# Optimization experiments

Measured on AMD Instinct MI355X. Metric: run time of the kernel, lower is better.

The kernel has to match this reference:

```python
import jax, jax.numpy as jnp
import numpy as np

# Module hyperparameters (from init_kwargs)
KH, KW = 3, 3
STRIDE_H = STRIDE_W = 1
PAD_H = PAD_W = 1
DIL_H = DIL_W = 1
DEFORM_GROUPS = 1
IN_CH, OUT_CH = 64, 64


def setup_inputs() -> dict:
    key = jax.random.key(0)
    k1, k2, k3, k4 = jax.random.split(key, 4)
    B, C, H, W = 4, IN_CH, 128, 128
    K = KH * KW
    x = jax.random.normal(k1, (B, C, H, W), dtype=jnp.float32)
    offset = jax.random.normal(k2, (B, DEFORM_GROUPS * 2 * K, H, W), dtype=jnp.float32)
    mask = jax.random.uniform(k3, (B, DEFORM_GROUPS * K, H, W), dtype=jnp.float32)
    stdv = 1.0 / np.sqrt(C * KH * KW)
    weight = jax.random.uniform(k4, (OUT_CH, C, KH, KW), dtype=jnp.float32,
                                minval=-stdv, maxval=stdv)
    bias = jnp.zeros((OUT_CH,), dtype=jnp.float32)
    return {"x": x, "offset": offset, "mask": mask, "weight": weight, "bias": bias}


def _bilinear_gather(img, ys, xs):
    """img: [N,Cg,H,W]; ys,xs: [N,K,Ho,Wo] absolute pixel coords.
    Returns [N,K,Ho,Wo,Cg]; zero padding outside, matches torch grid_sample
    (align_corners=False, padding_mode='zeros')."""
    N, Cg, H, W = img.shape
    y0f = jnp.floor(ys)
    x0f = jnp.floor(xs)
    wy = (ys - y0f)[..., None]
    wx = (xs - x0f)[..., None]
    y0 = y0f.astype(jnp.int32)
    x0 = x0f.astype(jnp.int32)
    b = jnp.arange(N)[:, None, None, None]

    def g(yi, xi):
        valid = (yi >= 0) & (yi < H) & (xi >= 0) & (xi < W)
        v = img[b, :, jnp.clip(yi, 0, H - 1), jnp.clip(xi, 0, W - 1)]  # [N,K,Ho,Wo,Cg]
        return jnp.where(valid[..., None], v, jnp.zeros((), img.dtype))

    v00 = g(y0, x0)
    v01 = g(y0, x0 + 1)
    v10 = g(y0 + 1, x0)
    v11 = g(y0 + 1, x0 + 1)
    return (v00 * (1 - wy) * (1 - wx) + v01 * (1 - wy) * wx
            + v10 * wy * (1 - wx) + v11 * wy * wx)


def _mdcn(x, offset, mask, weight, bias):
    B, C, H, W = x.shape
    O = weight.shape[0]
    K = KH * KW
    G = DEFORM_GROUPS
    Cg = C // G
    Ho = (H + 2 * PAD_H - (DIL_H * (KH - 1) + 1)) // STRIDE_H + 1
    Wo = (W + 2 * PAD_W - (DIL_W * (KW - 1) + 1)) // STRIDE_W + 1

    base_y = jnp.arange(Ho, dtype=x.dtype) * STRIDE_H - PAD_H          # [Ho]
    base_x = jnp.arange(Wo, dtype=x.dtype) * STRIDE_W - PAD_W          # [Wo]
    ky = (jnp.arange(K) // KW).astype(x.dtype) * DIL_H                 # [K]
    kx = (jnp.arange(K) % KW).astype(x.dtype) * DIL_W                  # [K]

    off = offset.reshape(B, G, K, 2, Ho, Wo)
    sy = (base_y[None, None, None, :, None] + ky[None, None, :, None, None]
          + off[:, :, :, 0])                                           # [B,G,K,Ho,Wo]
    sx = (base_x[None, None, None, None, :] + kx[None, None, :, None, None]
          + off[:, :, :, 1])

    img = x.reshape(B * G, Cg, H, W)
    sampled = _bilinear_gather(img, sy.reshape(B * G, K, Ho, Wo),
                               sx.reshape(B * G, K, Ho, Wo))            # [B*G,K,Ho,Wo,Cg]
    sampled = sampled * mask.reshape(B * G, K, Ho, Wo)[..., None]
    sampled = sampled.reshape(B, G, K, Ho, Wo, Cg)

    w = weight.reshape(O, G, Cg, K)
    out = jnp.einsum('bgkhwc,ogck->bohw', sampled, w)
    return out + bias[None, :, None, None]


def reference(x, offset, mask, weight, bias):
    return _mdcn(x, offset, mask, weight, bias)
```

## Files before the change

### kernel.cpp

```cpp
#include <hip/hip_runtime.h>
#include <hip/hip_bf16.h>
#include <math.h>

constexpr int B = 4, C = 64, H = 128, W = 128, K = 9, O = 64;
constexpr int HXW = H * W;

typedef _Float16 half8 __attribute__((ext_vector_type(8)));
typedef float f32x4 __attribute__((ext_vector_type(4)));

__global__ void wt_kernel(const float* __restrict__ weight, float* __restrict__ wt) {
    int idx = blockIdx.x * 256 + threadIdx.x;
    if (idx >= K * C * O) return;
    int o = idx & 63;
    int c = (idx >> 6) & 63;
    int k = idx >> 12;
    wt[idx] = weight[(o * C + c) * K + k];
}

__global__ __launch_bounds__(256) void mdcn_nchw(
        const float* __restrict__ x, const float* __restrict__ offset,
        const float* __restrict__ mask, const float* __restrict__ wt,
        const float* __restrict__ bias, float* __restrict__ out) {
    int pid = blockIdx.x * 256 + threadIdx.x;
    int b = pid >> 14;
    int hw = pid & (HXW - 1);
    int h = hw >> 7;
    int w = hw & 127;
    float acc[O];
#pragma unroll
    for (int o = 0; o < O; ++o) acc[o] = bias[o];
#pragma unroll 1
    for (int k = 0; k < K; ++k) {
        float offy = offset[((size_t)(b * 2 * K + 2 * k)) * HXW + hw];
        float offx = offset[((size_t)(b * 2 * K + 2 * k + 1)) * HXW + hw];
        float m    = mask[((size_t)(b * K + k)) * HXW + hw];
        float sy = (float)(h - 1 + k / 3) + offy;
        float sx = (float)(w - 1 + k % 3) + offx;
        float y0f = floorf(sy), x0f = floorf(sx);
        float wy = sy - y0f, wx = sx - x0f;
        int y0 = (int)y0f, x0 = (int)x0f;
        int y1 = y0 + 1, x1 = x0 + 1;
        bool vy0 = (y0 >= 0) & (y0 < H), vy1 = (y1 >= 0) & (y1 < H);
        bool vx0 = (x0 >= 0) & (x0 < W), vx1 = (x1 >= 0) & (x1 < W);
        float w00 = (vy0 & vx0) ? (1.0f - wy) * (1.0f - wx) * m : 0.0f;
        float w01 = (vy0 & vx1) ? (1.0f - wy) * wx * m : 0.0f;
        float w10 = (vy1 & vx0) ? wy * (1.0f - wx) * m : 0.0f;
        float w11 = (vy1 & vx1) ? wy * wx * m : 0.0f;
        int y0c = min(max(y0, 0), H - 1), y1c = min(max(y1, 0), H - 1);
        int x0c = min(max(x0, 0), W - 1), x1c = min(max(x1, 0), W - 1);
        const float* p00 = x + (size_t)b * C * HXW + y0c * W + x0c;
        const float* p01 = x + (size_t)b * C * HXW + y0c * W + x1c;
        const float* p10 = x + (size_t)b * C * HXW + y1c * W + x0c;
        const float* p11 = x + (size_t)b * C * HXW + y1c * W + x1c;
        const float* wk = wt + k * C * O;
#pragma unroll 1
        for (int c0 = 0; c0 < C; c0 += 4) {
            float v[4];
#pragma unroll
            for (int j = 0; j < 4; ++j) {
                size_t cs = (size_t)(c0 + j) * HXW;
                v[j] = w00 * p00[cs] + w01 * p01[cs] + w10 * p10[cs] + w11 * p11[cs];
            }
            const float* wr = wk + c0 * O;
#pragma unroll
            for (int j = 0; j < 4; ++j)
#pragma unroll
                for (int o = 0; o < O; ++o) acc[o] = fmaf(wr[j * O + o], v[j], acc[o]);
        }
    }
#pragma unroll
    for (int o = 0; o < O; ++o) out[((size_t)(b * O + o)) * HXW + hw] = acc[o];
}

constexpr int XT_BLOCKS = B * HXW / 128;
__global__ __launch_bounds__(256) void prep_kernel(
        const float* __restrict__ x, const float* __restrict__ weight,
        _Float16* __restrict__ xht, _Float16* __restrict__ wth) {
    int bid = blockIdx.x;
    if (bid < XT_BLOCKS) {
        __shared__ float lds[128 * 65];
        int t = threadIdx.x;
        int P = bid * 128;
        int b = P >> 14;
        int hw0 = P & (HXW - 1);
        int px = t & 127;
        int hf = t >> 7;
        const float* src = x + (size_t)b * C * HXW + hw0 + px;
#pragma unroll
        for (int cc = 0; cc < 32; ++cc) {
            int ch = hf * 32 + cc;
            lds[px * 65 + ch] = src[(size_t)ch * HXW];
        }
        __syncthreads();
        _Float16* dst = xht + ((size_t)b * HXW + hw0 + px) * 64 + hf * 32;
        const float* row = lds + px * 65 + hf * 32;
#pragma unroll
        for (int j = 0; j < 4; ++j) {
            half8 pk;
#pragma unroll
            for (int e = 0; e < 8; ++e) pk[e] = (_Float16)row[j * 8 + e];
            *(half8*)(dst + j * 8) = pk;
        }
    } else {
        int idx = (bid - XT_BLOCKS) * 256 + threadIdx.x;
        if (idx < K * O * C) {
            int e = idx & 7;
            int lane = (idx >> 3) & 63;
            int s = (idx >> 9) & 7;
            int k = idx >> 12;
            int ml = lane & 15, kg = lane >> 4;
            int nf = s & 3, ks = s >> 2;
            int o = nf * 16 + ml;
            int c = ks * 32 + kg * 8 + e;
            wth[idx] = (_Float16)weight[(o * C + c) * K + k];
        }
    }
}

__global__ __launch_bounds__(256, 4) void mdcn_f16(
        const _Float16* __restrict__ xht,
        const float* __restrict__ offset,
        const float* __restrict__ mask,
        const _Float16* __restrict__ wth,
        const float* __restrict__ bias,
        float* __restrict__ out) {
    __shared__ _Float16 Alds[4][16 * 64];

    int bid = blockIdx.x;
    int slab = bid & 7;
    int within = bid >> 3;
    int tid = threadIdx.x;
    int lane = tid & 63;
    int wid = tid >> 6;
    int ml = lane & 15, kg = lane >> 4;
    int p8 = lane >> 3, ch8 = lane & 7;
    int b = slab >> 1;
    int hwbase = (slab & 1) * 8192 + within * 64;
    int h = hwbase >> 7;
    int wvpx = wid * 16;
    int wbase = (hwbase & 127) + wvpx;
    _Float16* Aw = &Alds[wid][0];

    f32x4 acc[4];
#pragma unroll
    for (int nf = 0; nf < 4; ++nf) {
        float bv = bias[nf * 16 + ml];
        acc[nf] = (f32x4){bv, bv, bv, bv};
    }

    const _Float16* xb = xht + (size_t)b * HXW * 64;
    const float* offb = offset + (size_t)b * 2 * K * HXW;
    const float* mskb = mask + (size_t)b * K * HXW;

    float oy[2], ox[2], mm[2];
#pragma unroll
    for (int g = 0; g < 2; ++g) {
        int hw = hwbase + wvpx + g * 8 + p8;
        oy[g] = offb[hw];
        ox[g] = offb[(size_t)HXW + hw];
        mm[g] = mskb[hw];
    }

#pragma unroll 1
    for (int k = 0; k < K; ++k) {
        int ky = k / 3 - 1, kx = k % 3 - 1;

        float w00[2], w01[2], w10[2], w11[2];
        int r00[2], r01[2], r10[2], r11[2];
#pragma unroll
        for (int g = 0; g < 2; ++g) {
            int pl = g * 8 + p8;
            int w = wbase + pl;
            float sy = (float)(h + ky) + oy[g];
            float sx = (float)(w + kx) + ox[g];
            float y0f = floorf(sy), x0f = floorf(sx);
            float wy = sy - y0f, wx = sx - x0f;
            int y0 = (int)y0f, x0 = (int)x0f;
            int y1 = y0 + 1, x1 = x0 + 1;
            bool vy0 = (y0 >= 0) & (y0 < H), vy1 = (y1 >= 0) & (y1 < H);
            bool vx0 = (x0 >= 0) & (x0 < W), vx1 = (x1 >= 0) & (x1 < W);
            float m = mm[g];
            w00[g] = (vy0 & vx0) ? (1.0f - wy) * (1.0f - wx) * m : 0.0f;
            w01[g] = (vy0 & vx1) ? (1.0f - wy) * wx * m : 0.0f;
            w10[g] = (vy1 & vx0) ? wy * (1.0f - wx) * m : 0.0f;
            w11[g] = (vy1 & vx1) ? wy * wx * m : 0.0f;
            int y0c = min(max(y0, 0), H - 1), y1c = min(max(y1, 0), H - 1);
            int x0c = min(max(x0, 0), W - 1), x1c = min(max(x1, 0), W - 1);
            r00[g] = y0c * W + x0c;
            r01[g] = y0c * W + x1c;
            r10[g] = y1c * W + x0c;
            r11[g] = y1c * W + x1c;
        }

        half8 c00[2], c01[2], c10[2], c11[2];
#pragma unroll
        for (int g = 0; g < 2; ++g) {
            c00[g] = *(const half8*)(xb + r00[g] * 64 + ch8 * 8);
            c01[g] = *(const half8*)(xb + r01[g] * 64 + ch8 * 8);
            c10[g] = *(const half8*)(xb + r10[g] * 64 + ch8 * 8);
            c11[g] = *(const half8*)(xb + r11[g] * 64 + ch8 * 8);
        }

        float oy2[2], ox2[2], mm2[2];
        if (k + 1 < K) {
#pragma unroll
            for (int g = 0; g < 2; ++g) {
                int hw = hwbase + wvpx + g * 8 + p8;
                oy2[g] = offb[(size_t)(2 * k + 2) * HXW + hw];
                ox2[g] = offb[(size_t)(2 * k + 3) * HXW + hw];
                mm2[g] = mskb[(size_t)(k + 1) * HXW + hw];
            }
        }
        __builtin_amdgcn_sched_barrier(0);

#pragma unroll
        for (int g = 0; g < 2; ++g) {
            int pl = g * 8 + p8;
            _Float16 h00 = (_Float16)w00[g], h01 = (_Float16)w01[g];
            _Float16 h10 = (_Float16)w10[g], h11 = (_Float16)w11[g];
            half8 pk = c00[g] * h00 + c01[g] * h01 + c10[g] * h10 + c11[g] * h11;
            *(half8*)(Aw + pl * 64 + ((ch8 ^ (pl & 7)) * 8)) = pk;
        }

#pragma unroll
        for (int ks = 0; ks < 2; ++ks) {
            half8 bfr[4];
#pragma unroll
            for (int nf = 0; nf < 4; ++nf)
                bfr[nf] = *(const half8*)(wth + ((size_t)((k * 8 + ks * 4 + nf) * 64 + lane)) * 8);
            half8 af = *(const half8*)(Aw + ml * 64 + (((ks * 4 + kg) ^ (ml & 7)) * 8));
#pragma unroll
            for (int nf = 0; nf < 4; ++nf)
                acc[nf] = __builtin_amdgcn_mfma_f32_16x16x32_f16(af, bfr[nf], acc[nf], 0, 0, 0);
        }

        if (k + 1 < K) {
#pragma unroll
            for (int g = 0; g < 2; ++g) { oy[g] = oy2[g]; ox[g] = ox2[g]; mm[g] = mm2[g]; }
        }
    }

    int hwb = hwbase + wvpx + kg * 4;
#pragma unroll
    for (int nf = 0; nf < 4; ++nf) {
        size_t ob = ((size_t)(b * O + nf * 16 + ml)) * HXW + hwb;
        *(float4*)(out + ob) = __builtin_bit_cast(float4, acc[nf]);
    }
}

extern "C" void kernel_launch(void* const* d_in, const int* in_sizes, int n_in,
                              void* d_out, int out_size, void* d_ws, size_t ws_size,
                              hipStream_t stream) {
    const float* x      = (const float*)d_in[0];
    const float* offset = (const float*)d_in[1];
    const float* mask   = (const float*)d_in[2];
    const float* weight = (const float*)d_in[3];
    const float* bias   = (const float*)d_in[4];
    float* out = (float*)d_out;

    _Float16* wth = (_Float16*)d_ws;
    _Float16* xht = (_Float16*)((char*)d_ws + 73728);
    size_t need = 73728 + (size_t)B * HXW * 64 * sizeof(_Float16);

    if (ws_size >= need) {
        int wth_blocks = (K * O * C + 255) / 256;
        prep_kernel<<<XT_BLOCKS + wth_blocks, 256, 0, stream>>>(x, weight, xht, wth);
        mdcn_f16<<<1024, 256, 0, stream>>>(xht, offset, mask, wth, bias, out);
    } else {
        float* wt = (float*)d_ws;
        wt_kernel<<<(K * C * O + 255) / 256, 256, 0, stream>>>(weight, wt);
        mdcn_nchw<<<(B * HXW) / 256, 256, 0, stream>>>(x, offset, mask, wt, bias, out);
    }
}
```

Before: 39.42 us.

## Stage all weights in LDS and build MFMA A fragments in registers

Each 512-thread block now copies the full fp16 weight tensor (72KB) into shared memory once and reads B fragments from LDS instead of global memory. The per-wave LDS round trip for the sampled A tile is removed: each lane computes bilinear coordinates for its own pixel and gathers the channel slices that match its MFMA A-fragment layout directly. Blocks now cover a whole 128-pixel row, with half as many blocks of twice the size. The trade-offs are 72KB of LDS per block, which limits occupancy, and a prologue that loads every weight per block. Each pixel's coordinate math is also repeated across four lanes.

```diff
diff --git a/kernel.cpp b/kernel.cpp
--- a/kernel.cpp
+++ b/kernel.cpp
@@ -117,14 +117,14 @@
     }
 }
 
-__global__ __launch_bounds__(256, 4) void mdcn_f16(
+__global__ __launch_bounds__(512, 4) void mdcn_f16(
         const _Float16* __restrict__ xht,
         const float* __restrict__ offset,
         const float* __restrict__ mask,
         const _Float16* __restrict__ wth,
         const float* __restrict__ bias,
         float* __restrict__ out) {
-    __shared__ _Float16 Alds[4][16 * 64];
+    __shared__ _Float16 Wlds[K * 8 * 64 * 8];
 
     int bid = blockIdx.x;
     int slab = bid & 7;
@@ -133,13 +133,20 @@
     int lane = tid & 63;
     int wid = tid >> 6;
     int ml = lane & 15, kg = lane >> 4;
-    int p8 = lane >> 3, ch8 = lane & 7;
     int b = slab >> 1;
-    int hwbase = (slab & 1) * 8192 + within * 64;
-    int h = hwbase >> 7;
+    int row = (slab & 1) * 64 + within;
+    int hwrow = row * 128;
     int wvpx = wid * 16;
-    int wbase = (hwbase & 127) + wvpx;
-    _Float16* Aw = &Alds[wid][0];
+    int h = row;
+    int hwpx = hwrow + wvpx + ml;
+    int wpx = wvpx + ml;
+
+#pragma unroll
+    for (int j = 0; j < 9; ++j) {
+        int idx = tid + j * 512;
+        *(half8*)(Wlds + idx * 8) = *(const half8*)(wth + idx * 8);
+    }
+    __syncthreads();
 
     f32x4 acc[4];
 #pragma unroll
@@ -152,95 +159,70 @@
     const float* offb = offset + (size_t)b * 2 * K * HXW;
     const float* mskb = mask + (size_t)b * K * HXW;
 
-    float oy[2], ox[2], mm[2];
-#pragma unroll
-    for (int g = 0; g < 2; ++g) {
-        int hw = hwbase + wvpx + g * 8 + p8;
-        oy[g] = offb[hw];
-        ox[g] = offb[(size_t)HXW + hw];
-        mm[g] = mskb[hw];
-    }
+    float oy = offb[hwpx];
+    float ox = offb[(size_t)HXW + hwpx];
+    float mm = mskb[hwpx];
 
 #pragma unroll 1
     for (int k = 0; k < K; ++k) {
         int ky = k / 3 - 1, kx = k % 3 - 1;
 
-        float w00[2], w01[2], w10[2], w11[2];
-        int r00[2], r01[2], r10[2], r11[2];
-#pragma unroll
-        for (int g = 0; g < 2; ++g) {
-            int pl = g * 8 + p8;
-            int w = wbase + pl;
-            float sy = (float)(h + ky) + oy[g];
-            float sx = (float)(w + kx) + ox[g];
-            float y0f = floorf(sy), x0f = floorf(sx);
-            float wy = sy - y0f, wx = sx - x0f;
-            int y0 = (int)y0f, x0 = (int)x0f;
-            int y1 = y0 + 1, x1 = x0 + 1;
-            bool vy0 = (y0 >= 0) & (y0 < H), vy1 = (y1 >= 0) & (y1 < H);
-            bool vx0 = (x0 >= 0) & (x0 < W), vx1 = (x1 >= 0) & (x1 < W);
-            float m = mm[g];
-            w00[g] = (vy0 & vx0) ? (1.0f - wy) * (1.0f - wx) * m : 0.0f;
-            w01[g] = (vy0 & vx1) ? (1.0f - wy) * wx * m : 0.0f;
-            w10[g] = (vy1 & vx0) ? wy * (1.0f - wx) * m : 0.0f;
-            w11[g] = (vy1 & vx1) ? wy * wx * m : 0.0f;
-            int y0c = min(max(y0, 0), H - 1), y1c = min(max(y1, 0), H - 1);
-            int x0c = min(max(x0, 0), W - 1), x1c = min(max(x1, 0), W - 1);
-            r00[g] = y0c * W + x0c;
-            r01[g] = y0c * W + x1c;
-            r10[g] = y1c * W + x0c;
-            r11[g] = y1c * W + x1c;
-        }
+        float sy = (float)(h + ky) + oy;
+        float sx = (float)(wpx + kx) + ox;
+        float y0f = floorf(sy), x0f = floorf(sx);
+        float wy = sy - y0f, wx = sx - x0f;
+        int y0 = (int)y0f, x0 = (int)x0f;
+        int y1 = y0 + 1, x1 = x0 + 1;
+        bool vy0 = (y0 >= 0) & (y0 < H), vy1 = (y1 >= 0) & (y1 < H);
+        bool vx0 = (x0 >= 0) & (x0 < W), vx1 = (x1 >= 0) & (x1 < W);
+        float w00 = (vy0 & vx0) ? (1.0f - wy) * (1.0f - wx) * mm : 0.0f;
+        float w01 = (vy0 & vx1) ? (1.0f - wy) * wx * mm : 0.0f;
+        float w10 = (vy1 & vx0) ? wy * (1.0f - wx) * mm : 0.0f;
+        float w11 = (vy1 & vx1) ? wy * wx * mm : 0.0f;
+        int y0c = min(max(y0, 0), H - 1), y1c = min(max(y1, 0), H - 1);
+        int x0c = min(max(x0, 0), W - 1), x1c = min(max(x1, 0), W - 1);
+        int r00 = y0c * W + x0c, r01 = y0c * W + x1c;
+        int r10 = y1c * W + x0c, r11 = y1c * W + x1c;
+        int chb = kg * 8;
 
         half8 c00[2], c01[2], c10[2], c11[2];
 #pragma unroll
-        for (int g = 0; g < 2; ++g) {
-            c00[g] = *(const half8*)(xb + r00[g] * 64 + ch8 * 8);
-            c01[g] = *(const half8*)(xb + r01[g] * 64 + ch8 * 8);
-            c10[g] = *(const half8*)(xb + r10[g] * 64 + ch8 * 8);
-            c11[g] = *(const half8*)(xb + r11[g] * 64 + ch8 * 8);
-        }
-
-        float oy2[2], ox2[2], mm2[2];
+        for (int ks = 0; ks < 2; ++ks) {
+            int co = ks * 32 + chb;
+            c00[ks] = *(const half8*)(xb + r00 * 64 + co);
+            c01[ks] = *(const half8*)(xb + r01 * 64 + co);
+            c10[ks] = *(const half8*)(xb + r10 * 64 + co);
+            c11[ks] = *(const half8*)(xb + r11 * 64 + co);
+        }
+
+        float oy2 = 0.f, ox2 = 0.f, mm2 = 0.f;
         if (k + 1 < K) {
-#pragma unroll
-            for (int g = 0; g < 2; ++g) {
-                int hw = hwbase + wvpx + g * 8 + p8;
-                oy2[g] = offb[(size_t)(2 * k + 2) * HXW + hw];
-                ox2[g] = offb[(size_t)(2 * k + 3) * HXW + hw];
-                mm2[g] = mskb[(size_t)(k + 1) * HXW + hw];
+            oy2 = offb[(size_t)(2 * k + 2) * HXW + hwpx];
+            ox2 = offb[(size_t)(2 * k + 3) * HXW + hwpx];
+            mm2 = mskb[(size_t)(k + 1) * HXW + hwpx];
+        }
+        __builtin_amdgcn_sched_barrier(0);
+
+        _Float16 h00 = (_Float16)w00, h01 = (_Float16)w01;
+        _Float16 h10 = (_Float16)w10, h11 = (_Float16)w11;
+        half8 af[2];
+#pragma unroll
+        for (int ks = 0; ks < 2; ++ks)
+            af[ks] = c00[ks] * h00 + c01[ks] * h01 + c10[ks] * h10 + c11[ks] * h11;
+
+#pragma unroll
+        for (int ks = 0; ks < 2; ++ks) {
+#pragma unroll
+            for (int nf = 0; nf < 4; ++nf) {
+                half8 bfr = *(const half8*)(Wlds + ((k * 8 + ks * 4 + nf) * 64 + lane) * 8);
+                acc[nf] = __builtin_amdgcn_mfma_f32_16x16x32_f16(af[ks], bfr, acc[nf], 0, 0, 0);
             }
         }
-        __builtin_amdgcn_sched_barrier(0);
-
-#pragma unroll
-        for (int g = 0; g < 2; ++g) {
-            int pl = g * 8 + p8;
-            _Float16 h00 = (_Float16)w00[g], h01 = (_Float16)w01[g];
-            _Float16 h10 = (_Float16)w10[g], h11 = (_Float16)w11[g];
-            half8 pk = c00[g] * h00 + c01[g] * h01 + c10[g] * h10 + c11[g] * h11;
-            *(half8*)(Aw + pl * 64 + ((ch8 ^ (pl & 7)) * 8)) = pk;
-        }
-
-#pragma unroll
-        for (int ks = 0; ks < 2; ++ks) {
-            half8 bfr[4];
-#pragma unroll
-            for (int nf = 0; nf < 4; ++nf)
-                bfr[nf] = *(const half8*)(wth + ((size_t)((k * 8 + ks * 4 + nf) * 64 + lane)) * 8);
-            half8 af = *(const half8*)(Aw + ml * 64 + (((ks * 4 + kg) ^ (ml & 7)) * 8));
-#pragma unroll
-            for (int nf = 0; nf < 4; ++nf)
-                acc[nf] = __builtin_amdgcn_mfma_f32_16x16x32_f16(af, bfr[nf], acc[nf], 0, 0, 0);
-        }
-
-        if (k + 1 < K) {
-#pragma unroll
-            for (int g = 0; g < 2; ++g) { oy[g] = oy2[g]; ox[g] = ox2[g]; mm[g] = mm2[g]; }
-        }
-    }
-
-    int hwb = hwbase + wvpx + kg * 4;
+
+        oy = oy2; ox = ox2; mm = mm2;
+    }
+
+    int hwb = hwrow + wvpx + kg * 4;
 #pragma unroll
     for (int nf = 0; nf < 4; ++nf) {
         size_t ob = ((size_t)(b * O + nf * 16 + ml)) * HXW + hwb;
@@ -265,7 +247,7 @@
     if (ws_size >= need) {
         int wth_blocks = (K * O * C + 255) / 256;
         prep_kernel<<<XT_BLOCKS + wth_blocks, 256, 0, stream>>>(x, weight, xht, wth);
-        mdcn_f16<<<1024, 256, 0, stream>>>(xht, offset, mask, wth, bias, out);
+        mdcn_f16<<<512, 512, 0, stream>>>(xht, offset, mask, wth, bias, out);
     } else {
         float* wt = (float*)d_ws;
         wt_kernel<<<(K * C * O + 255) / 256, 256, 0, stream>>>(weight, wt);
```

Result: slower. 51.34 us (+30.2%).
